# Optimization experiments

Hardware: AMD Instinct MI355X
Metric: run time of the kernel (lower is better)

The kernel has to match this reference:

```python
import jax, jax.numpy as jnp
import numpy as np

NEG_SLOPE = 0.01  # LeakyReLU default


def gcn_conv(x, src, dst, W, b, num_nodes):
    """PyG GCNConv: x' = D^-1/2 (A+I) D^-1/2 (x W) + b, self-loops added."""
    h = x @ W
    loop = jnp.arange(num_nodes)
    s = jnp.concatenate([src, loop])
    d = jnp.concatenate([dst, loop])
    deg = jax.ops.segment_sum(jnp.ones(s.shape[0], dtype=h.dtype), d,
                              num_segments=num_nodes)
    dinv = jnp.where(deg > 0, jax.lax.rsqrt(deg), 0.0)
    norm = dinv[s] * dinv[d]              # (Ep+N,)
    out = jax.ops.segment_sum(h[s] * norm[:, None], d, num_segments=num_nodes)
    return out + b


def leaky_relu(x):
    return jnp.where(x > 0, x, NEG_SLOPE * x)


def setup_inputs() -> dict:
    key = jax.random.key(0)
    ks = jax.random.split(key, 8)
    B, V, E, Fsub, H = 16, 100000, 300000, 800000, 16
    verts = jax.random.normal(ks[0], (B, V, 3), dtype=jnp.float32)
    edges = jax.random.randint(ks[1], (E, 2), 0, V)
    faces_sub = jax.random.randint(ks[2], (Fsub, 3), 0, V + E)
    W1 = jax.random.normal(ks[3], (3, H), dtype=jnp.float32) * 0.01
    W2 = jax.random.normal(ks[4], (H, H), dtype=jnp.float32) * 0.01
    W3 = jax.random.normal(ks[5], (H, 3), dtype=jnp.float32) * 0.01
    return {"verts": verts, "edges": edges, "faces_sub": faces_sub,
            "W1": W1, "b1": jnp.zeros((H,), jnp.float32),
            "W2": W2, "b2": jnp.zeros((H,), jnp.float32),
            "W3": W3, "b3": jnp.zeros((3,), jnp.float32)}


def reference(verts, edges, faces_sub, W1, b1, W2, b2, W3, b3):
    B, V, _ = verts.shape
    E = edges.shape[0]
    N = B * V
    # pack edges across the batch (same topology per mesh, offset per mesh)
    offsets = (jnp.arange(B) * V).astype(edges.dtype)
    pe = (edges[None, :, :] + offsets[:, None, None]).reshape(B * E, 2)
    src, dst = pe[:, 0], pe[:, 1]

    x = verts.reshape(N, 3)
    h = leaky_relu(gcn_conv(x, src, dst, W1, b1, N))
    h = leaky_relu(gcn_conv(h, src, dst, W2, b2, N))
    # Dropout(0.5) is identity at inference
    offs = gcn_conv(h, src, dst, W3, b3, N)

    v = (x + offs).reshape(B, V, 3)          # offset_verts
    mid = v[:, edges].mean(axis=2)           # (B, E, 3) edge midpoints
    new_verts = jnp.concatenate([v, mid], axis=1)   # (B, V+E, 3)
    new_faces = jnp.broadcast_to(faces_sub[None], (B,) + faces_sub.shape)
    return new_verts, new_faces
```

## Files before the change

### kernel.cpp

```cpp
#include <hip/hip_runtime.h>
#include <hip/hip_bf16.h>

#define NEG_SLOPE 0.01f

typedef long long i64;
typedef __hip_bfloat16 bf16;

__device__ __forceinline__ float lrelu(float x) { return x > 0.f ? x : NEG_SLOPE * x; }
__device__ __forceinline__ float b2f(bf16 v) { return __bfloat162float(v); }
__device__ __forceinline__ float lo2f(unsigned u) { return __uint_as_float(u << 16); }
__device__ __forceinline__ float hi2f(unsigned u) { return __uint_as_float(u & 0xffff0000u); }
__device__ __forceinline__ unsigned pk2(float a, float b) {
    unsigned ua = __bfloat16_as_ushort(__float2bfloat16(a));
    unsigned ub = __bfloat16_as_ushort(__float2bfloat16(b));
    return ua | (ub << 16);
}
__device__ __forceinline__ void acc8(float* h, uint4 u) {
    h[0] += lo2f(u.x); h[1] += hi2f(u.x);
    h[2] += lo2f(u.y); h[3] += hi2f(u.y);
    h[4] += lo2f(u.z); h[5] += hi2f(u.z);
    h[6] += lo2f(u.w); h[7] += hi2f(u.w);
}

__device__ __forceinline__ void decode_bxb(int wg, int NB, int CBc, int& b, int& xb) {
    if ((CBc & 7) == 0) {
        int xcd = wg & 7, k = wg >> 3;
        int bl = k / NB;
        xb = k - bl * NB;
        b = xcd + 8 * bl;
    } else {
        b = wg / NB;
        xb = wg - b * NB;
    }
}

__global__ __launch_bounds__(256) void k_deg(const int* __restrict__ edges,
                                             int* __restrict__ indeg, int E) {
    int e = blockIdx.x * 256 + threadIdx.x;
    if (e < E) atomicAdd(&indeg[edges[2 * e + 1]], 1);
}

__global__ __launch_bounds__(256) void k_scan1(const int* __restrict__ indeg,
                                               int* __restrict__ rowptr,
                                               int* __restrict__ bsum,
                                               float* __restrict__ dinv, int V) {
    __shared__ int s[256];
    int i = blockIdx.x * 256 + threadIdx.x;
    int x = (i < V) ? indeg[i] : 0;
    if (i < V) dinv[i] = rsqrtf((float)x + 1.0f);
    s[threadIdx.x] = x;
    __syncthreads();
    for (int off = 1; off < 256; off <<= 1) {
        int t = (threadIdx.x >= (unsigned)off) ? s[threadIdx.x - off] : 0;
        __syncthreads();
        s[threadIdx.x] += t;
        __syncthreads();
    }
    if (i < V) rowptr[i] = s[threadIdx.x] - x;
    if (threadIdx.x == 255) bsum[blockIdx.x] = s[255];
}

__global__ __launch_bounds__(1024) void k_scan2(int* __restrict__ bsum, int NB) {
    __shared__ int s[1024];
    __shared__ int srun;
    if (threadIdx.x == 0) srun = 0;
    __syncthreads();
    for (int base = 0; base < NB; base += 1024) {
        int i = base + threadIdx.x;
        int x = (i < NB) ? bsum[i] : 0;
        s[threadIdx.x] = x;
        __syncthreads();
        for (int off = 1; off < 1024; off <<= 1) {
            int t = (threadIdx.x >= (unsigned)off) ? s[threadIdx.x - off] : 0;
            __syncthreads();
            s[threadIdx.x] += t;
            __syncthreads();
        }
        int run = srun;
        if (i < NB) bsum[i] = run + s[threadIdx.x] - x;
        __syncthreads();
        if (threadIdx.x == 1023) srun = run + s[1023];
        __syncthreads();
    }
}

__global__ __launch_bounds__(256) void k_scan3(int* __restrict__ rowptr,
                                               const int* __restrict__ bsum,
                                               int V, int E) {
    int i = blockIdx.x * 256 + threadIdx.x;
    if (i < V) rowptr[i] += bsum[blockIdx.x];
    if (i == 0) rowptr[V] = E;
}

__global__ __launch_bounds__(256) void k_rp2(const int* __restrict__ rowptr,
                                             int2* __restrict__ rp2, int V) {
    int v = blockIdx.x * 256 + threadIdx.x;
    if (v < V) rp2[v] = make_int2(rowptr[v], rowptr[v + 1]);
}

__global__ __launch_bounds__(256) void k_fill(const int* __restrict__ edges,
                                              const int* __restrict__ rowptr,
                                              int* __restrict__ cur,
                                              int* __restrict__ col, int E) {
    int e = blockIdx.x * 256 + threadIdx.x;
    if (e >= E) return;
    int s = edges[2 * e], d = edges[2 * e + 1];
    int p = atomicAdd(&cur[d], 1);
    col[rowptr[d] + p] = s;
}

__global__ __launch_bounds__(256) void k_gl12(const int2* __restrict__ rp2,
                                              const int* __restrict__ col,
                                              const float* __restrict__ verts,
                                              const float* __restrict__ W1,
                                              const float* __restrict__ b1,
                                              const float* __restrict__ W2,
                                              const float* __restrict__ dinv,
                                              bf16* __restrict__ PB,
                                              float* __restrict__ Q,
                                              int b0, int V, int NB, int CBc) {
    int b, xb;
    decode_bxb(blockIdx.x, NB, CBc, b, xb);
    int v = xb * 256 + threadIdx.x;
    if (v >= V) return;
    i64 vg = (i64)(b0 + b) * V;
    i64 vb = (i64)b * V;
    float di = dinv[v];
    const float* xv = verts + (vg + v) * 3;
    float c0 = di * xv[0], c1 = di * xv[1], c2 = di * xv[2];
    int2 r = rp2[v];
    int j = r.x;
    for (; j + 1 < r.y; j += 2) {
        int s0 = col[j], s1 = col[j + 1];
        float d0 = dinv[s0], d1 = dinv[s1];
        const float* p0 = verts + (vg + s0) * 3;
        const float* p1 = verts + (vg + s1) * 3;
        c0 += d0 * p0[0] + d1 * p1[0];
        c1 += d0 * p0[1] + d1 * p1[1];
        c2 += d0 * p0[2] + d1 * p1[2];
    }
    if (j < r.y) {
        int s0 = col[j];
        float d0 = dinv[s0];
        const float* p0 = verts + (vg + s0) * 3;
        c0 += d0 * p0[0]; c1 += d0 * p0[1]; c2 += d0 * p0[2];
    }
    float h[16];
#pragma unroll
    for (int f = 0; f < 16; ++f)
        h[f] = lrelu(di * (c0 * W1[f] + c1 * W1[16 + f] + c2 * W1[32 + f]) + b1[f]);
    float g[16];
#pragma unroll
    for (int f = 0; f < 16; ++f) g[f] = 0.f;
#pragma unroll
    for (int k = 0; k < 16; ++k) {
        float hk = h[k];
#pragma unroll
        for (int f = 0; f < 16; ++f) g[f] += hk * W2[k * 16 + f];
    }
#pragma unroll
    for (int f = 0; f < 16; ++f) g[f] *= di;
    i64 m = vb + v;
    uint4* Pp = (uint4*)(PB + m * 16);
    Pp[0] = make_uint4(pk2(g[0], g[1]), pk2(g[2], g[3]), pk2(g[4], g[5]), pk2(g[6], g[7]));
    Pp[1] = make_uint4(pk2(g[8], g[9]), pk2(g[10], g[11]), pk2(g[12], g[13]), pk2(g[14], g[15]));
    float4* Qp = (float4*)(Q + m * 16);
#pragma unroll
    for (int q = 0; q < 4; ++q)
        Qp[q] = make_float4(g[4 * q], g[4 * q + 1], g[4 * q + 2], g[4 * q + 3]);
}

__global__ __launch_bounds__(256) void k_gl3(const int2* __restrict__ rp2,
                                             const int* __restrict__ col,
                                             const float* __restrict__ W3,
                                             const float* __restrict__ b2,
                                             const float* __restrict__ dinv,
                                             const bf16* __restrict__ Pin,
                                             const float* __restrict__ Q,
                                             float* __restrict__ R,
                                             int V, int NB, int CBc) {
    int b, xb;
    decode_bxb(blockIdx.x, NB, CBc, b, xb);
    int v = xb * 256 + threadIdx.x;
    if (v >= V) return;
    i64 vb = (i64)b * V;
    i64 m = vb + v;
    float h[16];
    const float4* Qin = (const float4*)(Q + m * 16);
#pragma unroll
    for (int q = 0; q < 4; ++q) {
        float4 t = Qin[q];
        h[4 * q] = t.x; h[4 * q + 1] = t.y; h[4 * q + 2] = t.z; h[4 * q + 3] = t.w;
    }
    const uint4* Pb = (const uint4*)(Pin + vb * 16);
    int2 r = rp2[v];
    int j = r.x;
    for (; j + 1 < r.y; j += 2) {
        size_t u0 = (size_t)col[j] * 2, u1 = (size_t)col[j + 1] * 2;
        uint4 q0 = Pb[u0], q1 = Pb[u0 + 1];
        uint4 c0 = Pb[u1], c1 = Pb[u1 + 1];
        acc8(h, q0); acc8(h + 8, q1);
        acc8(h, c0); acc8(h + 8, c1);
    }
    if (j < r.y) {
        size_t u0 = (size_t)col[j] * 2;
        uint4 q0 = Pb[u0], q1 = Pb[u0 + 1];
        acc8(h, q0); acc8(h + 8, q1);
    }
    float di = dinv[v];
    float g0 = 0.f, g1 = 0.f, g2 = 0.f;
#pragma unroll
    for (int k = 0; k < 16; ++k) {
        float hk = lrelu(di * h[k] + b2[k]);
        g0 += hk * W3[k * 3 + 0];
        g1 += hk * W3[k * 3 + 1];
        g2 += hk * W3[k * 3 + 2];
    }
    ((float4*)R)[m] = make_float4(di * g0, di * g1, di * g2, 0.f);
}

__global__ __launch_bounds__(256) void k_gvert(const int2* __restrict__ rp2,
                                               const int* __restrict__ col,
                                               const float* __restrict__ x,
                                               const float* __restrict__ b3,
                                               const float* __restrict__ dinv,
                                               const float* __restrict__ R,
                                               float* __restrict__ Vpos,
                                               float* __restrict__ out0,
                                               int b0, int V, int E, int NB, int CBc) {
    int b, xb;
    decode_bxb(blockIdx.x, NB, CBc, b, xb);
    int v = xb * 256 + threadIdx.x;
    if (v >= V) return;
    i64 vb = (i64)b * V;
    i64 m = vb + v;
    const float4* Rb = (const float4*)R + vb;
    float4 s = Rb[v];
    int2 r = rp2[v];
    int j = r.x;
    for (; j + 1 < r.y; j += 2) {
        float4 t0 = Rb[col[j]];
        float4 t1 = Rb[col[j + 1]];
        s.x += t0.x + t1.x; s.y += t0.y + t1.y; s.z += t0.z + t1.z;
    }
    if (j < r.y) {
        float4 t0 = Rb[col[j]];
        s.x += t0.x; s.y += t0.y; s.z += t0.z;
    }
    float di = dinv[v];
    int bg = b0 + b;
    i64 n = (i64)bg * V + v;
    float p0 = x[n * 3]     + di * s.x + b3[0];
    float p1 = x[n * 3 + 1] + di * s.y + b3[1];
    float p2 = x[n * 3 + 2] + di * s.z + b3[2];
    ((float4*)Vpos)[m] = make_float4(p0, p1, p2, 0.f);
    i64 o = ((i64)bg * (V + E) + v) * 3;
    __builtin_nontemporal_store(p0, out0 + o);
    __builtin_nontemporal_store(p1, out0 + o + 1);
    __builtin_nontemporal_store(p2, out0 + o + 2);
}

__global__ __launch_bounds__(256) void k_mid(const int* __restrict__ edges,
                                             const float* __restrict__ Vpos,
                                             float* __restrict__ out0,
                                             int b0, int V, int E, int NB, int CBc) {
    int b, xe;
    decode_bxb(blockIdx.x, NB, CBc, b, xe);
    int e = xe * 256 + threadIdx.x;
    if (e >= E) return;
    int2 sd = ((const int2*)edges)[e];
    float4 ps = ((const float4*)Vpos)[(i64)b * V + sd.x];
    float4 pd = ((const float4*)Vpos)[(i64)b * V + sd.y];
    i64 o = ((i64)(b0 + b) * (V + E) + V + e) * 3;
    __builtin_nontemporal_store(0.5f * (ps.x + pd.x), out0 + o);
    __builtin_nontemporal_store(0.5f * (ps.y + pd.y), out0 + o + 1);
    __builtin_nontemporal_store(0.5f * (ps.z + pd.z), out0 + o + 2);
}

__global__ __launch_bounds__(256) void k_faces(const int* __restrict__ faces,
                                               float* __restrict__ out1,
                                               i64 F3, i64 faceElems) {
    i64 i = (i64)blockIdx.x * 256 + threadIdx.x;
    if (i >= F3) return;
    i64 o = (i64)blockIdx.y * F3 + i;
    if (o < faceElems) __builtin_nontemporal_store((float)faces[i], out1 + o);
}

__global__ __launch_bounds__(256) void k_faces4(const int4* __restrict__ faces4,
                                                float* __restrict__ out1,
                                                i64 Fq, i64 F3) {
    i64 t = (i64)blockIdx.x * 256 + threadIdx.x;
    if (t >= Fq) return;
    int4 u = faces4[t];
    float* p = out1 + (i64)blockIdx.y * F3 + t * 4;
    __builtin_nontemporal_store((float)u.x, p);
    __builtin_nontemporal_store((float)u.y, p + 1);
    __builtin_nontemporal_store((float)u.z, p + 2);
    __builtin_nontemporal_store((float)u.w, p + 3);
}

__global__ __launch_bounds__(256) void k_dinv_g(const int* __restrict__ indeg,
                                                float* __restrict__ dinv, int V) {
    int v = blockIdx.x * 256 + threadIdx.x;
    if (v < V) dinv[v] = rsqrtf((float)indeg[v] + 1.0f);
}

__global__ __launch_bounds__(256) void k_l1_g(const float* __restrict__ x,
                                              const float* __restrict__ W1,
                                              const float* __restrict__ dinv,
                                              bf16* __restrict__ P, float* __restrict__ Q,
                                              int b0, int V, int H) {
    extern __shared__ float sW[];
    for (int i = threadIdx.x; i < 3 * H; i += 256) sW[i] = W1[i];
    __syncthreads();
    int v = blockIdx.x * 256 + threadIdx.x;
    if (v >= V) return;
    i64 n = (i64)(b0 + blockIdx.y) * V + v;
    i64 m = (i64)blockIdx.y * V + v;
    float di = dinv[v];
    float x0 = x[n * 3], x1 = x[n * 3 + 1], x2 = x[n * 3 + 2];
    for (int f = 0; f < H; ++f) {
        float g = di * (x0 * sW[f] + x1 * sW[H + f] + x2 * sW[2 * H + f]);
        P[m * H + f] = __float2bfloat16(g);
        Q[m * H + f] = g;
    }
}

__global__ __launch_bounds__(256) void k_scatter_g(const int* __restrict__ edges,
                                                   const bf16* __restrict__ P,
                                                   float* __restrict__ Q,
                                                   int E, int V, int H) {
    int e = blockIdx.x * 256 + threadIdx.x;
    if (e >= E) return;
    int b = blockIdx.y;
    int s = edges[2 * e], d = edges[2 * e + 1];
    for (int f = 0; f < H; ++f)
        unsafeAtomicAdd(&Q[((i64)b * V + d) * H + f], b2f(P[((i64)b * V + s) * H + f]));
}

__global__ __launch_bounds__(256) void k_l2_g(const float* __restrict__ W2,
                                              const float* __restrict__ b1,
                                              const float* __restrict__ dinv,
                                              bf16* __restrict__ P, float* __restrict__ Q,
                                              int V, int H) {
    extern __shared__ float sW[];
    float* sb = sW + H * H;
    for (int i = threadIdx.x; i < H * H; i += 256) sW[i] = W2[i];
    for (int i = threadIdx.x; i < H; i += 256) sb[i] = b1[i];
    __syncthreads();
    int v = blockIdx.x * 256 + threadIdx.x;
    if (v >= V) return;
    i64 m = (i64)blockIdx.y * V + v;
    float di = dinv[v];
    float h[64];
    for (int k = 0; k < H; ++k) h[k] = lrelu(di * Q[m * H + k] + sb[k]);
    for (int f = 0; f < H; ++f) {
        float a = 0.f;
        for (int k = 0; k < H; ++k) a += h[k] * sW[k * H + f];
        float g = di * a;
        P[m * H + f] = __float2bfloat16(g);
        Q[m * H + f] = g;
    }
}

__global__ __launch_bounds__(256) void k_l3_g(const float* __restrict__ W3,
                                              const float* __restrict__ b2,
                                              const float* __restrict__ dinv,
                                              float* __restrict__ R,
                                              const float* __restrict__ Q, int V, int H) {
    extern __shared__ float sW[];
    float* sb = sW + H * 3;
    for (int i = threadIdx.x; i < H * 3; i += 256) sW[i] = W3[i];
    for (int i = threadIdx.x; i < H; i += 256) sb[i] = b2[i];
    __syncthreads();
    int v = blockIdx.x * 256 + threadIdx.x;
    if (v >= V) return;
    i64 m = (i64)blockIdx.y * V + v;
    float di = dinv[v];
    float g0 = 0.f, g1 = 0.f, g2 = 0.f;
    for (int k = 0; k < H; ++k) {
        float h = lrelu(di * Q[m * H + k] + sb[k]);
        g0 += h * sW[k * 3]; g1 += h * sW[k * 3 + 1]; g2 += h * sW[k * 3 + 2];
    }
    ((float4*)R)[m] = make_float4(di * g0, di * g1, di * g2, 0.f);
}

extern "C" void kernel_launch(void* const* d_in, const int* in_sizes, int n_in,
                              void* d_out, int out_size, void* d_ws, size_t ws_size,
                              hipStream_t stream) {
    const float* verts = (const float*)d_in[0];
    const int*   edges = (const int*)d_in[1];
    const int*   faces = (const int*)d_in[2];
    const float* W1 = (const float*)d_in[3];
    const float* b1 = (const float*)d_in[4];
    const float* W2 = (const float*)d_in[5];
    const float* b2 = (const float*)d_in[6];
    const float* W3 = (const float*)d_in[7];
    const float* b3 = (const float*)d_in[8];

    const i64 s0 = in_sizes[0];
    const i64 E  = in_sizes[1] / 2;
    const i64 F  = in_sizes[2] / 3;
    const int H  = in_sizes[4];
    i64 B = 0;
    const i64 denomB = 3 * (E + F);
    if ((i64)out_size > s0 && denomB > 0) {
        i64 Bc = ((i64)out_size - s0) / denomB;
        if (Bc >= 1 && s0 + Bc * denomB == (i64)out_size && s0 % (3 * Bc) == 0) B = Bc;
    }
    if (B == 0) {
        i64 num = (i64)out_size - s0 - 3 * F;
        if (num > 0 && E > 0 && num % (3 * E) == 0) {
            i64 Bc = num / (3 * E);
            if (Bc >= 1 && s0 % (3 * Bc) == 0) B = Bc;
        }
    }
    if (B == 0) B = 16;
    const i64 V = s0 / (3 * B);

    const i64 Vp  = (V + 255) & ~255LL;
    const i64 NB1 = Vp >> 8;
    const size_t AUX = (size_t)Vp * 4  + (size_t)Vp * 4
                     + (size_t)(Vp + 256) * 4
                     + (size_t)(NB1 + 256) * 4
                     + (size_t)Vp * 8
                     + (size_t)E * 4  + 1024;
    const size_t rowB = (size_t)(6 * H) + 96 + 64;
    i64 CB = B;
    while (CB > 1 && AUX + (size_t)CB * V * rowB + 8192 > ws_size) CB = (CB + 1) / 2;

    float* ws     = (float*)d_ws;
    float* dinv   = ws;
    int*   indeg  = (int*)(ws + Vp);
    int*   rowptr = indeg + Vp;
    int*   bsum   = rowptr + Vp + 256;
    int2*  rp2    = (int2*)(bsum + NB1 + 256);
    int*   col    = (int*)(rp2 + Vp);
    char*  base   = (char*)(((size_t)(col + E) + 255) & ~(size_t)255);
    auto pad = [](size_t x) { return (x + 255) & ~(size_t)255; };

    bf16 *PB = nullptr, *Pg = nullptr;
    float *Q, *R, *Vb;
    {
        char* p = base;
        if (H == 16) {
            PB = (bf16*)p;  p += pad((size_t)CB * V * 32);
            Q  = (float*)p; p += pad((size_t)CB * V * 64);
        } else {
            Pg = (bf16*)p;  p += pad((size_t)CB * V * 2 * H);
            Q  = (float*)p; p += pad((size_t)CB * V * 4 * H);
        }
        R  = (float*)p; p += pad((size_t)CB * V * 16);
        Vb = (float*)p;
    }

    const unsigned NBv = (unsigned)((V + 255) / 256);
    const unsigned NBe = (unsigned)((E + 255) / 256);

    hipMemsetAsync(indeg, 0, V * sizeof(int), stream);
    if (NBe) k_deg<<<dim3(NBe), 256, 0, stream>>>(edges, indeg, (int)E);
    k_scan1<<<dim3(NBv), 256, 0, stream>>>(indeg, rowptr, bsum, dinv, (int)V);
    k_scan2<<<dim3(1), 1024, 0, stream>>>(bsum, (int)NBv);
    k_scan3<<<dim3(NBv), 256, 0, stream>>>(rowptr, bsum, (int)V, (int)E);
    k_rp2<<<dim3(NBv), 256, 0, stream>>>(rowptr, rp2, (int)V);
    hipMemsetAsync(indeg, 0, V * sizeof(int), stream);
    if (NBe) k_fill<<<dim3(NBe), 256, 0, stream>>>(edges, rowptr, indeg, col, (int)E);

    float* out0 = (float*)d_out;
    const i64 vertElems = B * (V + E) * 3;
    float* out1 = out0 + vertElems;
    const i64 faceElems = (i64)out_size - vertElems;

    for (i64 b0 = 0; b0 < B; b0 += CB) {
        const i64 CBc = (B - b0 < CB) ? (B - b0) : CB;
        dim3 g1((unsigned)(NBv * CBc));
        dim3 g1e((unsigned)(NBe * CBc));
        if (H == 16) {
            k_gl12<<<g1, 256, 0, stream>>>(rp2, col, verts, W1, b1, W2, dinv,
                                           PB, Q, (int)b0, (int)V, (int)NBv, (int)CBc);
            k_gl3<<<g1, 256, 0, stream>>>(rp2, col, W3, b2, dinv, PB, Q, R,
                                          (int)V, (int)NBv, (int)CBc);
        } else {
            dim3 gn(NBv, (unsigned)CBc);
            dim3 ge(NBe, (unsigned)CBc);
            size_t sh1 = (size_t)3 * H * 4;
            size_t sh2 = ((size_t)H * H + H) * 4;
            size_t sh3 = ((size_t)H * 3 + H) * 4;
            k_l1_g<<<gn, 256, sh1, stream>>>(verts, W1, dinv, Pg, Q, (int)b0, (int)V, H);
            if (NBe) k_scatter_g<<<ge, 256, 0, stream>>>(edges, Pg, Q, (int)E, (int)V, H);
            k_l2_g<<<gn, 256, sh2, stream>>>(W2, b1, dinv, Pg, Q, (int)V, H);
            if (NBe) k_scatter_g<<<ge, 256, 0, stream>>>(edges, Pg, Q, (int)E, (int)V, H);
            k_l3_g<<<gn, 256, sh3, stream>>>(W3, b2, dinv, R, Q, (int)V, H);
        }
        k_gvert<<<g1, 256, 0, stream>>>(rp2, col, verts, b3, dinv, R, Vb, out0,
                                        (int)b0, (int)V, (int)E, (int)NBv, (int)CBc);
        if (NBe) k_mid<<<g1e, 256, 0, stream>>>(edges, Vb, out0, (int)b0, (int)V, (int)E,
                                                (int)NBe, (int)CBc);
    }
    const i64 F3 = 3 * F;
    if (faceElems > 0 && F3 > 0) {
        bool v4 = ((F3 & 3) == 0) && ((vertElems & 3) == 0) && (faceElems == B * F3);
        if (v4) {
            const i64 Fq = F3 >> 2;
            k_faces4<<<dim3((unsigned)((Fq + 255) / 256), (unsigned)B), 256, 0, stream>>>(
                (const int4*)faces, out1, Fq, F3);
        } else {
            k_faces<<<dim3((unsigned)((F3 + 255) / 256), (unsigned)B), 256, 0, stream>>>(
                faces, out1, F3, faceElems);
        }
    }
}
```

Baseline: 504.0 us.

## Sort vertices by in-degree to balance gather loops; loop batches in face copy

After: 551.6 us. 1.09x slower.

```diff
diff --git a/kernel.cpp b/kernel.cpp
--- a/kernel.cpp
+++ b/kernel.cpp
@@ -40,14 +40,84 @@
     if (e < E) atomicAdd(&indeg[edges[2 * e + 1]], 1);
 }
 
-__global__ __launch_bounds__(256) void k_scan1(const int* __restrict__ indeg,
+__global__ __launch_bounds__(256) void k_hist(const int* __restrict__ indeg,
+                                              int* __restrict__ hist, int V) {
+    __shared__ int lh[64];
+    if (threadIdx.x < 64) lh[threadIdx.x] = 0;
+    __syncthreads();
+    int v = blockIdx.x * 256 + threadIdx.x;
+    if (v < V) atomicAdd(&lh[min(indeg[v], 63)], 1);
+    __syncthreads();
+    if (threadIdx.x < 64 && lh[threadIdx.x]) atomicAdd(&hist[threadIdx.x], lh[threadIdx.x]);
+}
+
+__global__ __launch_bounds__(64) void k_hscan(const int* __restrict__ hist,
+                                              int* __restrict__ hbase,
+                                              int* __restrict__ hcnt) {
+    __shared__ int s[64];
+    int t = threadIdx.x;
+    int x = hist[t];
+    s[t] = x;
+    __syncthreads();
+    for (int off = 1; off < 64; off <<= 1) {
+        int u = (t >= off) ? s[t - off] : 0;
+        __syncthreads();
+        s[t] += u;
+        __syncthreads();
+    }
+    hbase[t] = s[t] - x;
+    hcnt[t] = 0;
+}
+
+__global__ __launch_bounds__(256) void k_place(const int* __restrict__ indeg,
+                                               const int* __restrict__ hbase,
+                                               int* __restrict__ hcnt,
+                                               int* __restrict__ slotOf,
+                                               int* __restrict__ sperm,
+                                               int* __restrict__ deg_p,
+                                               float* __restrict__ dinv_o,
+                                               float* __restrict__ dinv_p, int V) {
+    __shared__ int lh[64], lb[64];
+    if (threadIdx.x < 64) lh[threadIdx.x] = 0;
+    __syncthreads();
+    int v = blockIdx.x * 256 + threadIdx.x;
+    int d = 0, r = 0;
+    bool ok = v < V;
+    if (ok) { d = min(indeg[v], 63); r = atomicAdd(&lh[d], 1); }
+    __syncthreads();
+    if (threadIdx.x < 64)
+        lb[threadIdx.x] = lh[threadIdx.x] ? atomicAdd(&hcnt[threadIdx.x], lh[threadIdx.x]) : 0;
+    __syncthreads();
+    if (ok) {
+        int slot = hbase[d] + lb[d] + r;
+        slotOf[v] = slot;
+        sperm[slot] = v;
+        deg_p[slot] = indeg[v];
+        float di = rsqrtf((float)indeg[v] + 1.0f);
+        dinv_o[v] = di;
+        dinv_p[slot] = di;
+    }
+}
+
+__global__ __launch_bounds__(256) void k_ident(const int* __restrict__ indeg,
+                                               int* __restrict__ slotOf,
+                                               int* __restrict__ sperm,
+                                               int* __restrict__ deg_p,
+                                               float* __restrict__ dinv_o,
+                                               float* __restrict__ dinv_p, int V) {
+    int v = blockIdx.x * 256 + threadIdx.x;
+    if (v >= V) return;
+    slotOf[v] = v; sperm[v] = v; deg_p[v] = indeg[v];
+    float di = rsqrtf((float)indeg[v] + 1.0f);
+    dinv_o[v] = di; dinv_p[v] = di;
+}
+
+__global__ __launch_bounds__(256) void k_scan1(const int* __restrict__ degp,
                                                int* __restrict__ rowptr,
-                                               int* __restrict__ bsum,
-                                               float* __restrict__ dinv, int V) {
+                                               int* __restrict__ bsum, int V) {
     __shared__ int s[256];
     int i = blockIdx.x * 256 + threadIdx.x;
-    int x = (i < V) ? indeg[i] : 0;
-    if (i < V) dinv[i] = rsqrtf((float)x + 1.0f);
+    int x = (i < V) ? degp[i] : 0;
     s[threadIdx.x] = x;
     __syncthreads();
     for (int off = 1; off < 256; off <<= 1) {
@@ -98,24 +168,33 @@
     if (v < V) rp2[v] = make_int2(rowptr[v], rowptr[v + 1]);
 }
 
-__global__ __launch_bounds__(256) void k_fill(const int* __restrict__ edges,
-                                              const int* __restrict__ rowptr,
-                                              int* __restrict__ cur,
-                                              int* __restrict__ col, int E) {
+__global__ __launch_bounds__(256) void k_fill2(const int* __restrict__ edges,
+                                               const int* __restrict__ rowptr,
+                                               const int* __restrict__ slotOf,
+                                               int* __restrict__ cur,
+                                               int* __restrict__ col_o,
+                                               int* __restrict__ col_p,
+                                               int2* __restrict__ ep, int E) {
     int e = blockIdx.x * 256 + threadIdx.x;
     if (e >= E) return;
     int s = edges[2 * e], d = edges[2 * e + 1];
-    int p = atomicAdd(&cur[d], 1);
-    col[rowptr[d] + p] = s;
+    int ss = slotOf[s], ds = slotOf[d];
+    ep[e] = make_int2(ss, ds);
+    int p = atomicAdd(&cur[ds], 1);
+    int idx = rowptr[ds] + p;
+    col_o[idx] = s;
+    col_p[idx] = ss;
 }
 
 __global__ __launch_bounds__(256) void k_gl12(const int2* __restrict__ rp2,
-                                              const int* __restrict__ col,
+                                              const int* __restrict__ col_o,
+                                              const int* __restrict__ sperm,
                                               const float* __restrict__ verts,
                                               const float* __restrict__ W1,
                                               const float* __restrict__ b1,
                                               const float* __restrict__ W2,
-                                              const float* __restrict__ dinv,
+                                              const float* __restrict__ dinv_o,
+                                              const float* __restrict__ dinv_p,
                                               bf16* __restrict__ PB,
                                               float* __restrict__ Q,
                                               int b0, int V, int NB, int CBc) {
@@ -125,14 +204,14 @@
     if (v >= V) return;
     i64 vg = (i64)(b0 + b) * V;
     i64 vb = (i64)b * V;
-    float di = dinv[v];
-    const float* xv = verts + (vg + v) * 3;
+    float di = dinv_p[v];
+    const float* xv = verts + (vg + sperm[v]) * 3;
     float c0 = di * xv[0], c1 = di * xv[1], c2 = di * xv[2];
     int2 r = rp2[v];
     int j = r.x;
     for (; j + 1 < r.y; j += 2) {
-        int s0 = col[j], s1 = col[j + 1];
-        float d0 = dinv[s0], d1 = dinv[s1];
+        int s0 = col_o[j], s1 = col_o[j + 1];
+        float d0 = dinv_o[s0], d1 = dinv_o[s1];
         const float* p0 = verts + (vg + s0) * 3;
         const float* p1 = verts + (vg + s1) * 3;
         c0 += d0 * p0[0] + d1 * p1[0];
@@ -140,8 +219,8 @@
         c2 += d0 * p0[2] + d1 * p1[2];
     }
     if (j < r.y) {
-        int s0 = col[j];
-        float d0 = dinv[s0];
+        int s0 = col_o[j];
+        float d0 = dinv_o[s0];
         const float* p0 = verts + (vg + s0) * 3;
         c0 += d0 * p0[0]; c1 += d0 * p0[1]; c2 += d0 * p0[2];
     }
@@ -171,10 +250,10 @@
 }
 
 __global__ __launch_bounds__(256) void k_gl3(const int2* __restrict__ rp2,
-                                             const int* __restrict__ col,
+                                             const int* __restrict__ col_p,
                                              const float* __restrict__ W3,
                                              const float* __restrict__ b2,
-                                             const float* __restrict__ dinv,
+                                             const float* __restrict__ dinv_p,
                                              const bf16* __restrict__ Pin,
                                              const float* __restrict__ Q,
                                              float* __restrict__ R,
@@ -196,18 +275,18 @@
     int2 r = rp2[v];
     int j = r.x;
     for (; j + 1 < r.y; j += 2) {
-        size_t u0 = (size_t)col[j] * 2, u1 = (size_t)col[j + 1] * 2;
+        size_t u0 = (size_t)col_p[j] * 2, u1 = (size_t)col_p[j + 1] * 2;
         uint4 q0 = Pb[u0], q1 = Pb[u0 + 1];
         uint4 c0 = Pb[u1], c1 = Pb[u1 + 1];
         acc8(h, q0); acc8(h + 8, q1);
         acc8(h, c0); acc8(h + 8, c1);
     }
     if (j < r.y) {
-        size_t u0 = (size_t)col[j] * 2;
+        size_t u0 = (size_t)col_p[j] * 2;
         uint4 q0 = Pb[u0], q1 = Pb[u0 + 1];
         acc8(h, q0); acc8(h + 8, q1);
     }
-    float di = dinv[v];
+    float di = dinv_p[v];
     float g0 = 0.f, g1 = 0.f, g2 = 0.f;
 #pragma unroll
     for (int k = 0; k < 16; ++k) {
@@ -220,10 +299,11 @@
 }
 
 __global__ __launch_bounds__(256) void k_gvert(const int2* __restrict__ rp2,
-                                               const int* __restrict__ col,
+                                               const int* __restrict__ col_p,
+                                               const int* __restrict__ sperm,
                                                const float* __restrict__ x,
                                                const float* __restrict__ b3,
-                                               const float* __restrict__ dinv,
+                                               const float* __restrict__ dinv_p,
                                                const float* __restrict__ R,
                                                float* __restrict__ Vpos,
                                                float* __restrict__ out0,
@@ -239,28 +319,29 @@
     int2 r = rp2[v];
     int j = r.x;
     for (; j + 1 < r.y; j += 2) {
-        float4 t0 = Rb[col[j]];
-        float4 t1 = Rb[col[j + 1]];
+        float4 t0 = Rb[col_p[j]];
+        float4 t1 = Rb[col_p[j + 1]];
         s.x += t0.x + t1.x; s.y += t0.y + t1.y; s.z += t0.z + t1.z;
     }
     if (j < r.y) {
-        float4 t0 = Rb[col[j]];
+        float4 t0 = Rb[col_p[j]];
         s.x += t0.x; s.y += t0.y; s.z += t0.z;
     }
-    float di = dinv[v];
+    float di = dinv_p[v];
     int bg = b0 + b;
-    i64 n = (i64)bg * V + v;
+    int vo = sperm[v];
+    i64 n = (i64)bg * V + vo;
     float p0 = x[n * 3]     + di * s.x + b3[0];
     float p1 = x[n * 3 + 1] + di * s.y + b3[1];
     float p2 = x[n * 3 + 2] + di * s.z + b3[2];
     ((float4*)Vpos)[m] = make_float4(p0, p1, p2, 0.f);
-    i64 o = ((i64)bg * (V + E) + v) * 3;
-    __builtin_nontemporal_store(p0, out0 + o);
-    __builtin_nontemporal_store(p1, out0 + o + 1);
-    __builtin_nontemporal_store(p2, out0 + o + 2);
-}
-
-__global__ __launch_bounds__(256) void k_mid(const int* __restrict__ edges,
+    i64 o = ((i64)bg * (V + E) + vo) * 3;
+    out0[o]     = p0;
+    out0[o + 1] = p1;
+    out0[o + 2] = p2;
+}
+
+__global__ __launch_bounds__(256) void k_mid(const int2* __restrict__ ep,
                                              const float* __restrict__ Vpos,
                                              float* __restrict__ out0,
                                              int b0, int V, int E, int NB, int CBc) {
@@ -268,7 +349,7 @@
     decode_bxb(blockIdx.x, NB, CBc, b, xe);
     int e = xe * 256 + threadIdx.x;
     if (e >= E) return;
-    int2 sd = ((const int2*)edges)[e];
+    int2 sd = ep[e];
     float4 ps = ((const float4*)Vpos)[(i64)b * V + sd.x];
     float4 pd = ((const float4*)Vpos)[(i64)b * V + sd.y];
     i64 o = ((i64)(b0 + b) * (V + E) + V + e) * 3;
@@ -286,23 +367,20 @@
     if (o < faceElems) __builtin_nontemporal_store((float)faces[i], out1 + o);
 }
 
-__global__ __launch_bounds__(256) void k_faces4(const int4* __restrict__ faces4,
-                                                float* __restrict__ out1,
-                                                i64 Fq, i64 F3) {
+__global__ __launch_bounds__(256) void k_faces4b(const int4* __restrict__ faces4,
+                                                 float* __restrict__ out1,
+                                                 i64 Fq, i64 F3, int B) {
     i64 t = (i64)blockIdx.x * 256 + threadIdx.x;
     if (t >= Fq) return;
     int4 u = faces4[t];
-    float* p = out1 + (i64)blockIdx.y * F3 + t * 4;
-    __builtin_nontemporal_store((float)u.x, p);
-    __builtin_nontemporal_store((float)u.y, p + 1);
-    __builtin_nontemporal_store((float)u.z, p + 2);
-    __builtin_nontemporal_store((float)u.w, p + 3);
-}
-
-__global__ __launch_bounds__(256) void k_dinv_g(const int* __restrict__ indeg,
-                                                float* __restrict__ dinv, int V) {
-    int v = blockIdx.x * 256 + threadIdx.x;
-    if (v < V) dinv[v] = rsqrtf((float)indeg[v] + 1.0f);
+    float a = (float)u.x, b = (float)u.y, c = (float)u.z, d = (float)u.w;
+    for (int bb = 0; bb < B; ++bb) {
+        float* p = out1 + (i64)bb * F3 + t * 4;
+        __builtin_nontemporal_store(a, p);
+        __builtin_nontemporal_store(b, p + 1);
+        __builtin_nontemporal_store(c, p + 2);
+        __builtin_nontemporal_store(d, p + 3);
+    }
 }
 
 __global__ __launch_bounds__(256) void k_l1_g(const float* __restrict__ x,
@@ -420,23 +498,33 @@
 
     const i64 Vp  = (V + 255) & ~255LL;
     const i64 NB1 = Vp >> 8;
-    const size_t AUX = (size_t)Vp * 4  + (size_t)Vp * 4
+    const size_t AUX = (size_t)Vp * 4 * 6
                      + (size_t)(Vp + 256) * 4
                      + (size_t)(NB1 + 256) * 4
+                     + 192 * 4
                      + (size_t)Vp * 8
-                     + (size_t)E * 4  + 1024;
+                     + (size_t)E * 16  + 4096;
     const size_t rowB = (size_t)(6 * H) + 96 + 64;
     i64 CB = B;
     while (CB > 1 && AUX + (size_t)CB * V * rowB + 8192 > ws_size) CB = (CB + 1) / 2;
 
     float* ws     = (float*)d_ws;
-    float* dinv   = ws;
-    int*   indeg  = (int*)(ws + Vp);
-    int*   rowptr = indeg + Vp;
+    float* dinv_o = ws;
+    float* dinv_p = ws + Vp;
+    int*   indeg  = (int*)(ws + 2 * Vp);
+    int*   slotOf = indeg + Vp;
+    int*   sperm  = slotOf + Vp;
+    int*   deg_p  = sperm + Vp;
+    int*   rowptr = deg_p + Vp;
     int*   bsum   = rowptr + Vp + 256;
-    int2*  rp2    = (int2*)(bsum + NB1 + 256);
-    int*   col    = (int*)(rp2 + Vp);
-    char*  base   = (char*)(((size_t)(col + E) + 255) & ~(size_t)255);
+    int*   hist   = bsum + NB1 + 256;
+    int*   hbase  = hist + 64;
+    int*   hcnt   = hbase + 64;
+    int2*  rp2    = (int2*)(((size_t)(hcnt + 64) + 15) & ~(size_t)15);
+    int2*  ep     = rp2 + Vp;
+    int*   col_o  = (int*)(ep + E);
+    int*   col_p  = col_o + E;
+    char*  base   = (char*)(((size_t)(col_p + E) + 255) & ~(size_t)255);
     auto pad = [](size_t x) { return (x + 255) & ~(size_t)255; };
 
     bf16 *PB = nullptr, *Pg = nullptr;
@@ -459,12 +547,23 @@
 
     hipMemsetAsync(indeg, 0, V * sizeof(int), stream);
     if (NBe) k_deg<<<dim3(NBe), 256, 0, stream>>>(edges, indeg, (int)E);
-    k_scan1<<<dim3(NBv), 256, 0, stream>>>(indeg, rowptr, bsum, dinv, (int)V);
+    if (H == 16) {
+        hipMemsetAsync(hist, 0, 64 * sizeof(int), stream);
+        k_hist<<<dim3(NBv), 256, 0, stream>>>(indeg, hist, (int)V);
+        k_hscan<<<dim3(1), 64, 0, stream>>>(hist, hbase, hcnt);
+        k_place<<<dim3(NBv), 256, 0, stream>>>(indeg, hbase, hcnt, slotOf, sperm,
+                                               deg_p, dinv_o, dinv_p, (int)V);
+    } else {
+        k_ident<<<dim3(NBv), 256, 0, stream>>>(indeg, slotOf, sperm, deg_p,
+                                               dinv_o, dinv_p, (int)V);
+    }
+    k_scan1<<<dim3(NBv), 256, 0, stream>>>(deg_p, rowptr, bsum, (int)V);
     k_scan2<<<dim3(1), 1024, 0, stream>>>(bsum, (int)NBv);
     k_scan3<<<dim3(NBv), 256, 0, stream>>>(rowptr, bsum, (int)V, (int)E);
     k_rp2<<<dim3(NBv), 256, 0, stream>>>(rowptr, rp2, (int)V);
     hipMemsetAsync(indeg, 0, V * sizeof(int), stream);
-    if (NBe) k_fill<<<dim3(NBe), 256, 0, stream>>>(edges, rowptr, indeg, col, (int)E);
+    if (NBe) k_fill2<<<dim3(NBe), 256, 0, stream>>>(edges, rowptr, slotOf, indeg,
+                                                    col_o, col_p, ep, (int)E);
 
     float* out0 = (float*)d_out;
     const i64 vertElems = B * (V + E) * 3;
@@ -476,9 +575,10 @@
         dim3 g1((unsigned)(NBv * CBc));
         dim3 g1e((unsigned)(NBe * CBc));
         if (H == 16) {
-            k_gl12<<<g1, 256, 0, stream>>>(rp2, col, verts, W1, b1, W2, dinv,
-                                           PB, Q, (int)b0, (int)V, (int)NBv, (int)CBc);
-            k_gl3<<<g1, 256, 0, stream>>>(rp2, col, W3, b2, dinv, PB, Q, R,
+            k_gl12<<<g1, 256, 0, stream>>>(rp2, col_o, sperm, verts, W1, b1, W2,
+                                           dinv_o, dinv_p, PB, Q,
+                                           (int)b0, (int)V, (int)NBv, (int)CBc);
+            k_gl3<<<g1, 256, 0, stream>>>(rp2, col_p, W3, b2, dinv_p, PB, Q, R,
                                           (int)V, (int)NBv, (int)CBc);
         } else {
             dim3 gn(NBv, (unsigned)CBc);
@@ -486,15 +586,15 @@
             size_t sh1 = (size_t)3 * H * 4;
             size_t sh2 = ((size_t)H * H + H) * 4;
             size_t sh3 = ((size_t)H * 3 + H) * 4;
-            k_l1_g<<<gn, 256, sh1, stream>>>(verts, W1, dinv, Pg, Q, (int)b0, (int)V, H);
+            k_l1_g<<<gn, 256, sh1, stream>>>(verts, W1, dinv_o, Pg, Q, (int)b0, (int)V, H);
             if (NBe) k_scatter_g<<<ge, 256, 0, stream>>>(edges, Pg, Q, (int)E, (int)V, H);
-            k_l2_g<<<gn, 256, sh2, stream>>>(W2, b1, dinv, Pg, Q, (int)V, H);
+            k_l2_g<<<gn, 256, sh2, stream>>>(W2, b1, dinv_o, Pg, Q, (int)V, H);
             if (NBe) k_scatter_g<<<ge, 256, 0, stream>>>(edges, Pg, Q, (int)E, (int)V, H);
-            k_l3_g<<<gn, 256, sh3, stream>>>(W3, b2, dinv, R, Q, (int)V, H);
+            k_l3_g<<<gn, 256, sh3, stream>>>(W3, b2, dinv_o, R, Q, (int)V, H);
         }
-        k_gvert<<<g1, 256, 0, stream>>>(rp2, col, verts, b3, dinv, R, Vb, out0,
-                                        (int)b0, (int)V, (int)E, (int)NBv, (int)CBc);
-        if (NBe) k_mid<<<g1e, 256, 0, stream>>>(edges, Vb, out0, (int)b0, (int)V, (int)E,
+        k_gvert<<<g1, 256, 0, stream>>>(rp2, col_p, sperm, verts, b3, dinv_p, R, Vb,
+                                        out0, (int)b0, (int)V, (int)E, (int)NBv, (int)CBc);
+        if (NBe) k_mid<<<g1e, 256, 0, stream>>>(ep, Vb, out0, (int)b0, (int)V, (int)E,
                                                 (int)NBe, (int)CBc);
     }
     const i64 F3 = 3 * F;
@@ -502,8 +602,8 @@
         bool v4 = ((F3 & 3) == 0) && ((vertElems & 3) == 0) && (faceElems == B * F3);
         if (v4) {
             const i64 Fq = F3 >> 2;
-            k_faces4<<<dim3((unsigned)((Fq + 255) / 256), (unsigned)B), 256, 0, stream>>>(
-                (const int4*)faces, out1, Fq, F3);
+            k_faces4b<<<dim3((unsigned)((Fq + 255) / 256)), 256, 0, stream>>>(
+                (const int4*)faces, out1, Fq, F3, (int)B);
         } else {
             k_faces<<<dim3((unsigned)((F3 + 255) / 256), (unsigned)B), 256, 0, stream>>>(
                 faces, out1, F3, faceElems);
```
